# Optimization experiments

Hardware: AMD Instinct MI355X
Metric: run time of the kernel (lower is better)

Reference implementation:

```python
import jax, jax.numpy as jnp
import numpy as np

N_NODES = 50000
N_EDGES = 800000
F_IN = 128
HID = 128
F_ADD = 32
N_GRAPHS = 128


def setup_inputs() -> dict:
    key = jax.random.key(0)
    ks = jax.random.split(key, 12)
    x = jax.random.normal(ks[0], (N_NODES, F_IN), dtype=jnp.float32)
    edge_index = jax.random.randint(ks[1], (2, N_EDGES), 0, N_NODES, dtype=jnp.int64)
    batch = jnp.sort(jax.random.randint(ks[2], (N_NODES,), 0, N_GRAPHS, dtype=jnp.int64))
    additional_features = jax.random.normal(ks[3], (N_GRAPHS, F_ADD), dtype=jnp.float32)
    def glorot(k, shape):
        fan_in, fan_out = shape[0], shape[1]
        lim = jnp.sqrt(6.0 / (fan_in + fan_out)).astype(jnp.float32)
        return jax.random.uniform(k, shape, jnp.float32, -lim, lim)
    W1 = glorot(ks[4], (F_IN, HID)); b1 = jnp.zeros((HID,), jnp.float32)
    W2 = glorot(ks[5], (HID, HID)); b2 = jnp.zeros((HID,), jnp.float32)
    fc1_w = glorot(ks[6], (HID + F_ADD, HID)); fc1_b = jnp.zeros((HID,), jnp.float32)
    fc2_w = glorot(ks[7], (HID, 2)); fc2_b = jnp.zeros((2,), jnp.float32)
    return {"x": x, "edge_index": edge_index, "batch": batch,
            "additional_features": additional_features,
            "W1": W1, "b1": b1, "W2": W2, "b2": b2,
            "fc1_w": fc1_w, "fc1_b": fc1_b, "fc2_w": fc2_w, "fc2_b": fc2_b}


def _gcn_conv(h, src, dst, norm, W, b):
    # h: [N, d_in]; symmetric-normalized scatter-add aggregation (PyG GCNConv)
    h = h @ W                                   # [N, d_out]
    msg = h[src] * norm[:, None]                # gather + scale: [E+N, d_out]
    return jax.ops.segment_sum(msg, dst, num_segments=N_NODES) + b


def reference(x, edge_index, batch, additional_features,
              W1, b1, W2, b2, fc1_w, fc1_b, fc2_w, fc2_b):
    loops = jnp.arange(N_NODES, dtype=edge_index.dtype)
    src = jnp.concatenate([edge_index[0], loops])   # A + I
    dst = jnp.concatenate([edge_index[1], loops])
    deg = jax.ops.segment_sum(jnp.ones_like(src, dtype=x.dtype), dst,
                              num_segments=N_NODES)
    dinv = jnp.where(deg > 0, jax.lax.rsqrt(jnp.maximum(deg, 1.0)), 0.0)
    norm = dinv[src] * dinv[dst]

    h = jax.nn.relu(_gcn_conv(x, src, dst, norm, W1, b1))
    h = jax.nn.relu(_gcn_conv(h, src, dst, norm, W2, b2))
    # dropout is identity in eval mode

    sums = jax.ops.segment_sum(h, batch, num_segments=N_GRAPHS)    # [G, HID]
    counts = jax.ops.segment_sum(jnp.ones((N_NODES,), h.dtype), batch,
                                 num_segments=N_GRAPHS)
    pooled = sums / jnp.maximum(counts, 1.0)[:, None]              # global_mean_pool

    z = jnp.concatenate([pooled, additional_features], axis=1)     # [G, HID+F_ADD]
    z = jax.nn.relu(z @ fc1_w + fc1_b)
    return z @ fc2_w + fc2_b                                       # [G, 2]
```

## Files before the change

kernel.cpp:

```cpp
#include <hip/hip_runtime.h>

#define NN 50000
#define NE 800000
#define FD 128
#define FDH 64
#define FA 32
#define NG 128
#define EETOT (NE + NN)
#define NBLK ((NN + 255) / 256)
#define NPXCD 6250
#define ECHK 2048
#define NCHK ((NE + ECHK - 1) / ECHK)
#define FPB 52
#define FILLB (8 * FPB)
#define GEMMB ((NN + 63) / 64)

typedef __attribute__((ext_vector_type(8))) short short8;
typedef __attribute__((ext_vector_type(4))) float f32x4;

__device__ __forceinline__ float bfbits(unsigned short u) {
    return __uint_as_float(((unsigned int)u) << 16);
}
__device__ __forceinline__ float bflo(unsigned int p) { return __uint_as_float(p << 16); }
__device__ __forceinline__ float bfhi(unsigned int p) { return __uint_as_float(p & 0xffff0000u); }
__device__ __forceinline__ unsigned short f2bf(float f) {
    unsigned int u = __float_as_uint(f);
    unsigned int r = u + 0x7FFFu + ((u >> 16) & 1u);
    return (unsigned short)(r >> 16);
}
__device__ __forceinline__ unsigned int packbf(float a, float b) {
    return (unsigned int)f2bf(a) | ((unsigned int)f2bf(b) << 16);
}

__device__ __forceinline__ int wave_probe_bf16(const unsigned int* t, int nwords) {
    int lane = threadIdx.x & 63;
    unsigned int wv = (lane < nwords) ? t[lane] : 0u;
    int nzp = (wv != 0u) ? 1 : 0;
    unsigned int e = (wv >> 7) & 0xFFu;
    int hitp = (nzp && e >= 100u && e <= 140u) ? 1 : 0;
    int nz = __popcll(__ballot(nzp));
    int hits = __popcll(__ballot(hitp));
    return (nz < 8) ? 1 : (hits * 4 >= nz * 3);
}
__device__ __forceinline__ int wave_probe_is64(const int* ei) {
    int lane = threadIdx.x & 63;
    int v = (lane < 32) ? ei[2 * lane + 1] : 0;
    return (__ballot(v != 0) == 0ull) ? 1 : 0;
}

__global__ __launch_bounds__(128) void mark_kernel(float* out, float v) {
    out[threadIdx.x] = v;
}

__global__ __launch_bounds__(256) void prep(
        const void* addf, const void* w1, const void* b1, const void* w2,
        const void* b2, const void* fc1w, const void* fc1b, const void* fc2w,
        const void* fc2b, unsigned int* W1t, unsigned int* W2t,
        float* addff, float* b1f, float* b2f, float* fc1wf, float* fc1bf,
        float* fc2wf, float* fc2bf, int* degi, int* tsum) {
    int b = blockIdx.x;
    if (b < 64) {
        int rel = b * 256 + threadIdx.x;
        const void* src = (rel < 8192) ? w1 : w2;
        unsigned int* dst = (rel < 8192) ? W1t : W2t;
        int flag = wave_probe_bf16((const unsigned int*)src, 64);
        int rr = rel & 8191;
        int n = rr >> 6, kk = rr & 63;
        float lo, hi;
        if (flag) {
            const unsigned short* s = (const unsigned short*)src;
            lo = bfbits(s[(2 * kk) * FD + n]);
            hi = bfbits(s[(2 * kk + 1) * FD + n]);
        } else {
            const float* s = (const float*)src;
            lo = s[(2 * kk) * FD + n];
            hi = s[(2 * kk + 1) * FD + n];
        }
        dst[rr] = packbf(lo, hi);
    } else if (b < 163) {
        int i = (b - 64) * 256 + threadIdx.x;
        int wb = (b - 64) * 256 + (threadIdx.x & ~63);
        const void* src; float* dst; int base; int prnw; int lim;
        if      (wb < 4096)  { src = addf; dst = addff; base = 0;     prnw = 64; lim = 4096;  }
        else if (wb < 4224)  { src = b1;   dst = b1f;   base = 4096;  prnw = 64; lim = 128;   }
        else if (wb < 4352)  { src = b2;   dst = b2f;   base = 4224;  prnw = 64; lim = 128;   }
        else if (wb < 24832) { src = fc1w; dst = fc1wf; base = 4352;  prnw = 64; lim = 20480; }
        else if (wb < 24960) { src = fc1b; dst = fc1bf; base = 24832; prnw = 64; lim = 128;   }
        else if (wb < 25216) { src = fc2w; dst = fc2wf; base = 24960; prnw = 64; lim = 256;   }
        else if (wb < 25280) { src = fc2b; dst = fc2bf; base = 25216; prnw = 1;  lim = 2;     }
        else return;
        int flag = wave_probe_bf16((const unsigned int*)src, prnw);
        int rel = i - base;
        if (rel < lim) {
            if (flag) dst[rel] = bfbits(((const unsigned short*)src)[rel]);
            else      dst[rel] = ((const float*)src)[rel];
        }
    } else {
        int i = (b - 163) * 256 + threadIdx.x;
        if      (i < NN)       degi[i] = 0;
        else if (i < NN + 256) tsum[i - NN] = 0;
    }
}

__global__ __launch_bounds__(256) void bin_gemm1(const int* ei, int* deg,
        int2* ebsd, int* bofs,
        const void* __restrict__ Av, const unsigned int* __restrict__ Wt,
        unsigned short* __restrict__ C) {
    __shared__ unsigned int hA[64][68];
    if ((int)blockIdx.x < NCHK) {
        __shared__ int cnt[8];
        __shared__ int sbase[8];
        int is64 = wave_probe_is64(ei);
        int chunk = blockIdx.x;
        int e0 = chunk * ECHK;
        int nedge = NE - e0; if (nedge > ECHK) nedge = ECHK;
        if (threadIdx.x < 8) cnt[threadIdx.x] = 0;
        __syncthreads();
        int sA[8], dA[8], rk[8], pr[8];
        #pragma unroll
        for (int k = 0; k < 8; ++k) {
            int j = k * 256 + threadIdx.x;
            pr[k] = -1;
            if (j < nedge) {
                int e = e0 + j;
                int s = is64 ? ei[2 * e] : ei[e];
                int d = is64 ? ei[2 * (NE + e)] : ei[NE + e];
                atomicAdd(&deg[d], 1);
                int p = d / NPXCD;
                sA[k] = s; dA[k] = d; pr[k] = p;
                rk[k] = atomicAdd(&cnt[p], 1);
            }
        }
        __syncthreads();
        if (threadIdx.x == 0) {
            int acc = 0;
            #pragma unroll
            for (int p = 0; p < 8; ++p) {
                sbase[p] = acc;
                bofs[chunk * 8 + p] = acc;
                acc += cnt[p];
            }
        }
        __syncthreads();
        #pragma unroll
        for (int k = 0; k < 8; ++k) {
            if (pr[k] >= 0) {
                int idx = chunk * ECHK + sbase[pr[k]] + rk[k];
                ebsd[idx] = make_int2(sA[k], dA[k]);
            }
        }
        return;
    }
    int bid = blockIdx.x - NCHK;
    int mbase = bid * 64;
    bool f32in = !wave_probe_bf16((const unsigned int*)Av, 64);
    if (!f32in) {
        const unsigned int* xb = (const unsigned int*)Av;
        for (int i = threadIdx.x; i < 64 * 64; i += 256) {
            int row = i >> 6, w = i & 63;
            int gr = mbase + row; if (gr >= NN) gr = NN - 1;
            hA[row][w] = xb[(size_t)gr * 64 + w];
        }
    } else {
        const float2* xf2 = (const float2*)Av;
        for (int i = threadIdx.x; i < 64 * 64; i += 256) {
            int row = i >> 6, w = i & 63;
            int gr = mbase + row; if (gr >= NN) gr = NN - 1;
            float2 f = xf2[(size_t)gr * 64 + w];
            hA[row][w] = packbf(f.x, f.y);
        }
    }
    __syncthreads();
    int wave = threadIdx.x >> 6;
    int lane = threadIdx.x & 63;
    int quad = lane >> 4;
    int l16  = lane & 15;
    int lrow = wave * 16 + l16;
    short8 af[4];
    #pragma unroll
    for (int kk = 0; kk < 4; ++kk) {
        uint4 v = *(const uint4*)&hA[lrow][(kk * 4 + quad) * 4];
        af[kk] = *(short8*)&v;
    }
    __syncthreads();
    f32x4 accs[8];
    #pragma unroll
    for (int nt = 0; nt < 8; ++nt) {
        int n = nt * 16 + l16;
        const uint4* Wrow = (const uint4*)(Wt + (size_t)n * FDH);
        f32x4 acc = {0.f, 0.f, 0.f, 0.f};
        #pragma unroll
        for (int kk = 0; kk < 4; ++kk) {
            uint4 wv = Wrow[kk * 4 + quad];
            short8 bf = *(short8*)&wv;
            acc = __builtin_amdgcn_mfma_f32_16x16x32_bf16(af[kk], bf, acc, 0, 0, 0);
        }
        accs[nt] = acc;
    }
    unsigned short* hs = (unsigned short*)hA;
    #pragma unroll
    for (int nt = 0; nt < 8; ++nt) {
        #pragma unroll
        for (int reg = 0; reg < 4; ++reg) {
            int row = wave * 16 + quad * 4 + reg;
            hs[row * 136 + nt * 16 + l16] = f2bf(accs[nt][reg]);
        }
    }
    __syncthreads();
    for (int i = threadIdx.x; i < 64 * 32; i += 256) {
        int row = i >> 5, q = i & 31;
        int gr = mbase + row;
        if (gr < NN)
            ((uint2*)C)[(size_t)gr * 32 + q] = ((const uint2*)&hs[row * 136])[q];
    }
}

__global__ __launch_bounds__(256) void scan_fused(const int* degi, const int* batch,
        int* tsum, float* dinv, int* rowstart, int* cursor, int* gstart) {
    __shared__ int sh[256];
    int b = blockIdx.x, t = threadIdx.x;
    int i = b * 256 + t;
    int d = (i < NN) ? degi[i] : 0;
    if (i < NN) dinv[i] = rsqrtf((float)(d + 1));
    int v = (i < NN) ? d + 1 : 0;
    sh[t] = v;
    __syncthreads();
    for (int off = 1; off < 256; off <<= 1) {
        int a = (t >= off) ? sh[t - off] : 0;
        __syncthreads();
        sh[t] += a;
        __syncthreads();
    }
    int incl = sh[t];
    int total = sh[255];
    if (t == 0) atomicExch(&tsum[b], total);
    int pt = 0;
    for (int j = t; j < b; j += 256) {
        int s;
        do { s = atomicAdd(&tsum[j], 0); } while (s == 0);
        pt += s;
    }
    __syncthreads();
    sh[t] = pt;
    __syncthreads();
    for (int off = 128; off >= 1; off >>= 1) {
        if (t < off) sh[t] += sh[t + off];
        __syncthreads();
    }
    int boff = sh[0];
    if (i < NN) {
        int r = boff + incl - v;
        rowstart[i] = r;
        cursor[i]   = r;
    }
    if (i == 0) rowstart[NN] = EETOT;
    if (i < NN) {
        int is64 = (batch[NN - 1] == 0) ? 1 : 0;
        int bc = is64 ? batch[2 * i] : batch[i];
        if (i == 0) {
            for (int g = 0; g <= bc; ++g) gstart[g] = 0;
        } else {
            int bp = is64 ? batch[2 * (i - 1)] : batch[i - 1];
            for (int g = bp + 1; g <= bc; ++g) gstart[g] = i;
        }
        if (i == NN - 1) {
            for (int g = bc + 1; g <= NG; ++g) gstart[g] = NN;
        }
    }
}

__global__ __launch_bounds__(256) void fill_kernel(const int2* ebsd, const int* bofs,
        const float* dinv, int* cursor, unsigned int* cv) {
    int par = blockIdx.x & 7;
    int g   = blockIdx.x >> 3;
    for (int chunk = g; chunk < NCHK; chunk += FPB) {
        int b0 = bofs[chunk * 8 + par];
        int nedge = NE - chunk * ECHK; if (nedge > ECHK) nedge = ECHK;
        int b1 = (par < 7) ? bofs[chunk * 8 + par + 1] : nedge;
        for (int j = b0 + (int)threadIdx.x; j < b1; j += 256) {
            int2 sd = ebsd[chunk * ECHK + j];
            int pos = atomicAdd(&cursor[sd.y], 1);
            cv[pos] = (unsigned int)sd.x
                    | ((unsigned int)f2bf(dinv[sd.x] * dinv[sd.y]) << 16);
        }
    }
    for (int n = par * NPXCD + g * 256 + threadIdx.x; n < (par + 1) * NPXCD;
         n += FPB * 256) {
        int pos = atomicAdd(&cursor[n], 1);
        float di = dinv[n];
        cv[pos] = (unsigned int)n | ((unsigned int)f2bf(di * di) << 16);
    }
}

__global__ __launch_bounds__(256) void agg_gemm2(const unsigned int* Hb,
        const unsigned int* cv, const int* rowstart, const float* bias,
        const unsigned int* __restrict__ Wt, unsigned short* __restrict__ C) {
    __shared__ unsigned int hA[16][68];
    int lane = threadIdx.x & 63;
    int r4   = lane >> 4;
    int c4   = lane & 15;
    int wv   = threadIdx.x >> 6;
    int nb = blockIdx.x * 16;
    int n = nb + wv * 4 + r4;
    const uint4* H4 = (const uint4*)Hb;
    int jb = rowstart[n], je = rowstart[n + 1];
    float a0 = 0.f, a1 = 0.f, a2 = 0.f, a3 = 0.f;
    float a4 = 0.f, a5 = 0.f, a6 = 0.f, a7 = 0.f;
    int j = jb;
    for (; j + 7 < je; j += 8) {
        unsigned int rr[8]; uint4 hh[8];
        #pragma unroll
        for (int k = 0; k < 8; ++k) rr[k] = cv[j + k];
        #pragma unroll
        for (int k = 0; k < 8; ++k) hh[k] = H4[(size_t)(rr[k] & 0xFFFFu) * 16 + c4];
        #pragma unroll
        for (int k = 0; k < 8; ++k) {
            float v = bfbits((unsigned short)(rr[k] >> 16));
            a0 += v * bflo(hh[k].x); a1 += v * bfhi(hh[k].x);
            a2 += v * bflo(hh[k].y); a3 += v * bfhi(hh[k].y);
            a4 += v * bflo(hh[k].z); a5 += v * bfhi(hh[k].z);
            a6 += v * bflo(hh[k].w); a7 += v * bfhi(hh[k].w);
        }
    }
    for (; j + 3 < je; j += 4) {
        unsigned int rr[4]; uint4 hh[4];
        #pragma unroll
        for (int k = 0; k < 4; ++k) rr[k] = cv[j + k];
        #pragma unroll
        for (int k = 0; k < 4; ++k) hh[k] = H4[(size_t)(rr[k] & 0xFFFFu) * 16 + c4];
        #pragma unroll
        for (int k = 0; k < 4; ++k) {
            float v = bfbits((unsigned short)(rr[k] >> 16));
            a0 += v * bflo(hh[k].x); a1 += v * bfhi(hh[k].x);
            a2 += v * bflo(hh[k].y); a3 += v * bfhi(hh[k].y);
            a4 += v * bflo(hh[k].z); a5 += v * bfhi(hh[k].z);
            a6 += v * bflo(hh[k].w); a7 += v * bfhi(hh[k].w);
        }
    }
    for (; j < je; ++j) {
        unsigned int r = cv[j];
        uint4 h = H4[(size_t)(r & 0xFFFFu) * 16 + c4];
        float v = bfbits((unsigned short)(r >> 16));
        a0 += v * bflo(h.x); a1 += v * bfhi(h.x);
        a2 += v * bflo(h.y); a3 += v * bfhi(h.y);
        a4 += v * bflo(h.z); a5 += v * bfhi(h.z);
        a6 += v * bflo(h.w); a7 += v * bfhi(h.w);
    }
    a0 = fmaxf(a0 + bias[8 * c4 + 0], 0.f);
    a1 = fmaxf(a1 + bias[8 * c4 + 1], 0.f);
    a2 = fmaxf(a2 + bias[8 * c4 + 2], 0.f);
    a3 = fmaxf(a3 + bias[8 * c4 + 3], 0.f);
    a4 = fmaxf(a4 + bias[8 * c4 + 4], 0.f);
    a5 = fmaxf(a5 + bias[8 * c4 + 5], 0.f);
    a6 = fmaxf(a6 + bias[8 * c4 + 6], 0.f);
    a7 = fmaxf(a7 + bias[8 * c4 + 7], 0.f);
    int lrow = wv * 4 + r4;
    hA[lrow][c4 * 4 + 0] = packbf(a0, a1);
    hA[lrow][c4 * 4 + 1] = packbf(a2, a3);
    hA[lrow][c4 * 4 + 2] = packbf(a4, a5);
    hA[lrow][c4 * 4 + 3] = packbf(a6, a7);
    __syncthreads();
    int quad = lane >> 4;
    int l16  = lane & 15;
    short8 af[4];
    #pragma unroll
    for (int kk = 0; kk < 4; ++kk) {
        const uint4* p = (const uint4*)&hA[l16][(kk * 4 + quad) * 4];
        uint4 v = *p;
        af[kk] = *(short8*)&v;
    }
    #pragma unroll
    for (int t = 0; t < 2; ++t) {
        int nt = wv * 2 + t;
        int nn2 = nt * 16 + l16;
        const uint4* Wrow = (const uint4*)(Wt + (size_t)nn2 * FDH);
        f32x4 acc = {0.f, 0.f, 0.f, 0.f};
        #pragma unroll
        for (int kk = 0; kk < 4; ++kk) {
            uint4 wvv = Wrow[kk * 4 + quad];
            short8 bf = *(short8*)&wvv;
            acc = __builtin_amdgcn_mfma_f32_16x16x32_bf16(af[kk], bf, acc, 0, 0, 0);
        }
        int row0 = nb + quad * 4;
        #pragma unroll
        for (int reg = 0; reg < 4; ++reg) {
            int r = row0 + reg;
            C[(size_t)r * FD + nt * 16 + l16] = f2bf(acc[reg]);
        }
    }
}

__global__ __launch_bounds__(256) void aggregate_kernel(const unsigned int* Hb,
        const unsigned int* cv, const int* rowstart, const float* bias,
        unsigned int* outb) {
    int lane = threadIdx.x & 63;
    int r4   = lane >> 4;
    int c4   = lane & 15;
    int wv   = threadIdx.x >> 6;
    int n = blockIdx.x * 16 + wv * 4 + r4;
    const uint4* H4 = (const uint4*)Hb;
    int jb = rowstart[n], je = rowstart[n + 1];
    float a0 = 0.f, a1 = 0.f, a2 = 0.f, a3 = 0.f;
    float a4 = 0.f, a5 = 0.f, a6 = 0.f, a7 = 0.f;
    int j = jb;
    for (; j + 7 < je; j += 8) {
        unsigned int rr[8]; uint4 hh[8];
        #pragma unroll
        for (int k = 0; k < 8; ++k) rr[k] = cv[j + k];
        #pragma unroll
        for (int k = 0; k < 8; ++k) hh[k] = H4[(size_t)(rr[k] & 0xFFFFu) * 16 + c4];
        #pragma unroll
        for (int k = 0; k < 8; ++k) {
            float v = bfbits((unsigned short)(rr[k] >> 16));
            a0 += v * bflo(hh[k].x); a1 += v * bfhi(hh[k].x);
            a2 += v * bflo(hh[k].y); a3 += v * bfhi(hh[k].y);
            a4 += v * bflo(hh[k].z); a5 += v * bfhi(hh[k].z);
            a6 += v * bflo(hh[k].w); a7 += v * bfhi(hh[k].w);
        }
    }
    for (; j + 3 < je; j += 4) {
        unsigned int rr[4]; uint4 hh[4];
        #pragma unroll
        for (int k = 0; k < 4; ++k) rr[k] = cv[j + k];
        #pragma unroll
        for (int k = 0; k < 4; ++k) hh[k] = H4[(size_t)(rr[k] & 0xFFFFu) * 16 + c4];
        #pragma unroll
        for (int k = 0; k < 4; ++k) {
            float v = bfbits((unsigned short)(rr[k] >> 16));
            a0 += v * bflo(hh[k].x); a1 += v * bfhi(hh[k].x);
            a2 += v * bflo(hh[k].y); a3 += v * bfhi(hh[k].y);
            a4 += v * bflo(hh[k].z); a5 += v * bfhi(hh[k].z);
            a6 += v * bflo(hh[k].w); a7 += v * bfhi(hh[k].w);
        }
    }
    for (; j < je; ++j) {
        unsigned int r = cv[j];
        uint4 h = H4[(size_t)(r & 0xFFFFu) * 16 + c4];
        float v = bfbits((unsigned short)(r >> 16));
        a0 += v * bflo(h.x); a1 += v * bfhi(h.x);
        a2 += v * bflo(h.y); a3 += v * bfhi(h.y);
        a4 += v * bflo(h.z); a5 += v * bfhi(h.z);
        a6 += v * bflo(h.w); a7 += v * bfhi(h.w);
    }
    a0 = fmaxf(a0 + bias[8 * c4 + 0], 0.f);
    a1 = fmaxf(a1 + bias[8 * c4 + 1], 0.f);
    a2 = fmaxf(a2 + bias[8 * c4 + 2], 0.f);
    a3 = fmaxf(a3 + bias[8 * c4 + 3], 0.f);
    a4 = fmaxf(a4 + bias[8 * c4 + 4], 0.f);
    a5 = fmaxf(a5 + bias[8 * c4 + 5], 0.f);
    a6 = fmaxf(a6 + bias[8 * c4 + 6], 0.f);
    a7 = fmaxf(a7 + bias[8 * c4 + 7], 0.f);
    uint4 out;
    out.x = packbf(a0, a1);
    out.y = packbf(a2, a3);
    out.z = packbf(a4, a5);
    out.w = packbf(a6, a7);
    ((uint4*)outb)[(size_t)n * 16 + c4] = out;
}

__global__ __launch_bounds__(256) void poolhead(const unsigned int* Hb,
        const int* gstart, const float* addf, const float* fc1w, const float* fc1b,
        const float* fc2w, const float* fc2b, const unsigned int* x, void* outp) {
    int g = blockIdx.x;
    int t = threadIdx.x;
    int q = t >> 6, w = t & 63;
    int obf = wave_probe_bf16(x, 64);
    int s = gstart[g], e = gstart[g + 1];
    float a0 = 0.f, a1 = 0.f;
    #pragma unroll 4
    for (int n = s + q; n < e; n += 4) {
        unsigned int h = Hb[(size_t)n * FDH + w];
        a0 += bflo(h);
        a1 += bfhi(h);
    }
    __shared__ float pp[4][FD];
    __shared__ float z[FD + FA];
    __shared__ float h[FD];
    pp[q][2 * w]     = a0;
    pp[q][2 * w + 1] = a1;
    __syncthreads();
    if (t < FD) {
        float cnt = (float)(e - s);
        if (cnt < 1.0f) cnt = 1.0f;
        z[t] = (pp[0][t] + pp[1][t] + pp[2][t] + pp[3][t]) / cnt;
    }
    if (t >= FD && t < FD + FA) z[t] = addf[g * FA + (t - FD)];
    __syncthreads();
    if (t < FD) {
        float acc = fc1b[t];
        #pragma unroll 4
        for (int k = 0; k < FD + FA; ++k)
            acc += z[k] * fc1w[k * FD + t];
        h[t] = fmaxf(acc, 0.f);
    }
    __syncthreads();
    if (t < 2) {
        float o = fc2b[t];
        for (int j = 0; j < FD; ++j) o += h[j] * fc2w[j * 2 + t];
        if (obf) ((unsigned short*)outp)[g * 2 + t] = f2bf(o);
        else     ((float*)outp)[g * 2 + t] = o;
    }
}

extern "C" void kernel_launch(void* const* d_in, const int* in_sizes, int n_in,
                              void* d_out, int out_size, void* d_ws, size_t ws_size,
                              hipStream_t stream) {
    (void)out_size;

    if (n_in != 12) {
        hipLaunchKernelGGL(mark_kernel, dim3(1), dim3(128), 0, stream,
                           (float*)d_out, 2000.0f);
        return;
    }
    const int exp_sizes[12] = {6400000, 1600000, 50000, 4096, 16384, 128,
                               16384, 128, 20480, 128, 256, 2};
    for (int i = 0; i < 12; ++i) {
        if (in_sizes[i] != exp_sizes[i]) {
            hipLaunchKernelGGL(mark_kernel, dim3(1), dim3(128), 0, stream,
                               (float*)d_out, 3000.0f + 100.0f * i);
            return;
        }
    }

    size_t off = 0;
    char* base = (char*)d_ws;
#define WSALLOC(ptr, type, nbytes) \
    type* ptr = (type*)(base + off); off += (((size_t)(nbytes)) + 255) & ~(size_t)255;
    WSALLOC(bufA,  unsigned int, (size_t)NN * FDH * 4)
    WSALLOC(bufB,  unsigned int, (size_t)NN * FDH * 4)
    WSALLOC(dinv,  float, (size_t)NN * 4)
    WSALLOC(degi,  int,   (size_t)NN * 4)
    WSALLOC(tsum,  int,   256 * 4)
    WSALLOC(rowst, int,   (size_t)(NN + 1) * 4)
    WSALLOC(cursor,int,   (size_t)NN * 4)
    WSALLOC(cv,    unsigned int, (size_t)EETOT * 4)
    WSALLOC(gstart,int,   (size_t)(NG + 1) * 4)
    WSALLOC(ebsd,  int2,  (size_t)NCHK * ECHK * 8)
    WSALLOC(bofs,  int,   (size_t)NCHK * 8 * 4)
    WSALLOC(W1t,   unsigned int, (size_t)FD * FDH * 4)
    WSALLOC(W2t,   unsigned int, (size_t)FD * FDH * 4)
    WSALLOC(b1f,   float, FD * 4)
    WSALLOC(b2f,   float, FD * 4)
    WSALLOC(addff, float, (size_t)NG * FA * 4)
    WSALLOC(fc1wf, float, (size_t)(FD + FA) * FD * 4)
    WSALLOC(fc1bf, float, FD * 4)
    WSALLOC(fc2wf, float, FD * 2 * 4)
    WSALLOC(fc2bf, float, 2 * 4)
#undef WSALLOC
    if (ws_size < off) {
        hipLaunchKernelGGL(mark_kernel, dim3(1), dim3(128), 0, stream,
                           (float*)d_out, 1000.0f);
        return;
    }

    const int* ei    = (const int*)d_in[1];
    const int* batch = (const int*)d_in[2];

    hipLaunchKernelGGL(prep, dim3(360), dim3(256), 0, stream,
                       d_in[3], d_in[4], d_in[5], d_in[6], d_in[7],
                       d_in[8], d_in[9], d_in[10], d_in[11],
                       W1t, W2t, addff, b1f, b2f, fc1wf, fc1bf,
                       fc2wf, fc2bf, degi, tsum);

    hipLaunchKernelGGL(bin_gemm1, dim3(NCHK + GEMMB), dim3(256), 0, stream,
                       ei, degi, ebsd, bofs,
                       d_in[0], W1t, (unsigned short*)bufA);

    hipLaunchKernelGGL(scan_fused, dim3(NBLK), dim3(256), 0, stream,
                       degi, batch, tsum, dinv, rowst, cursor, gstart);

    hipLaunchKernelGGL(fill_kernel, dim3(FILLB), dim3(256), 0, stream,
                       ebsd, bofs, dinv, cursor, cv);

    hipLaunchKernelGGL(agg_gemm2, dim3(NN / 16), dim3(256), 0, stream,
                       bufA, cv, rowst, b1f, W2t, (unsigned short*)bufB);

    hipLaunchKernelGGL(aggregate_kernel, dim3(NN / 16), dim3(256), 0, stream,
                       bufB, cv, rowst, b2f, bufA);

    hipLaunchKernelGGL(poolhead, dim3(NG), dim3(256), 0, stream,
                       bufA, gstart, addff, fc1wf, fc1bf, fc2wf, fc2bf,
                       (const unsigned int*)d_in[0], d_out);
}
```

Before: 278.8 us.

## Move edge binning into prep kernel and count degrees from binned edges

Edge binning by destination partition now runs inside the prep kernel, and the degree histogram moves into the GEMM1 kernel. There, blocks walk the binned edge list one destination partition at a time, so each block's degree atomics land in a narrow, likely cache-local range instead of random addresses across all nodes. The cost is an extra read of the binned edge array in the second kernel. The prep launch also grows by the binning blocks, and the degree counters are zeroed in the same launch before the second kernel reads them.

```diff
diff --git a/kernel.cpp b/kernel.cpp
--- a/kernel.cpp
+++ b/kernel.cpp
@@ -14,6 +14,7 @@
 #define FPB 52
 #define FILLB (8 * FPB)
 #define GEMMB ((NN + 63) / 64)
+#define PREPB 360
 
 typedef __attribute__((ext_vector_type(8))) short short8;
 typedef __attribute__((ext_vector_type(4))) float f32x4;
@@ -52,12 +53,13 @@
     out[threadIdx.x] = v;
 }
 
-__global__ __launch_bounds__(256) void prep(
+__global__ __launch_bounds__(256) void prep_bin(
         const void* addf, const void* w1, const void* b1, const void* w2,
         const void* b2, const void* fc1w, const void* fc1b, const void* fc2w,
         const void* fc2b, unsigned int* W1t, unsigned int* W2t,
         float* addff, float* b1f, float* b2f, float* fc1wf, float* fc1bf,
-        float* fc2wf, float* fc2bf, int* degi, int* tsum) {
+        float* fc2wf, float* fc2bf, int* degi, int* tsum,
+        const int* ei, int2* ebsd, int* bofs) {
     int b = blockIdx.x;
     if (b < 64) {
         int rel = b * 256 + threadIdx.x;
@@ -77,6 +79,7 @@
             hi = s[(2 * kk + 1) * FD + n];
         }
         dst[rr] = packbf(lo, hi);
+        return;
     } else if (b < 163) {
         int i = (b - 64) * 256 + threadIdx.x;
         int wb = (b - 64) * 256 + (threadIdx.x & ~63);
@@ -95,63 +98,75 @@
             if (flag) dst[rel] = bfbits(((const unsigned short*)src)[rel]);
             else      dst[rel] = ((const float*)src)[rel];
         }
-    } else {
+        return;
+    } else if (b < PREPB) {
         int i = (b - 163) * 256 + threadIdx.x;
         if      (i < NN)       degi[i] = 0;
         else if (i < NN + 256) tsum[i - NN] = 0;
-    }
-}
-
-__global__ __launch_bounds__(256) void bin_gemm1(const int* ei, int* deg,
-        int2* ebsd, int* bofs,
+        return;
+    }
+    __shared__ int cnt[8];
+    __shared__ int sbase[8];
+    int is64 = wave_probe_is64(ei);
+    int chunk = b - PREPB;
+    int e0 = chunk * ECHK;
+    int nedge = NE - e0; if (nedge > ECHK) nedge = ECHK;
+    if (threadIdx.x < 8) cnt[threadIdx.x] = 0;
+    __syncthreads();
+    int sA[8], dA[8], rk[8], pr[8];
+    #pragma unroll
+    for (int k = 0; k < 8; ++k) {
+        int j = k * 256 + threadIdx.x;
+        pr[k] = -1;
+        if (j < nedge) {
+            int e = e0 + j;
+            int s = is64 ? ei[2 * e] : ei[e];
+            int d = is64 ? ei[2 * (NE + e)] : ei[NE + e];
+            int p = d / NPXCD;
+            sA[k] = s; dA[k] = d; pr[k] = p;
+            rk[k] = atomicAdd(&cnt[p], 1);
+        }
+    }
+    __syncthreads();
+    if (threadIdx.x == 0) {
+        int acc = 0;
+        #pragma unroll
+        for (int p = 0; p < 8; ++p) {
+            sbase[p] = acc;
+            bofs[chunk * 8 + p] = acc;
+            acc += cnt[p];
+        }
+    }
+    __syncthreads();
+    #pragma unroll
+    for (int k = 0; k < 8; ++k) {
+        if (pr[k] >= 0) {
+            int idx = chunk * ECHK + sbase[pr[k]] + rk[k];
+            ebsd[idx] = make_int2(sA[k], dA[k]);
+        }
+    }
+}
+
+__global__ __launch_bounds__(256) void deg_gemm1(const int2* ebsd, const int* bofs,
+        int* degi,
         const void* __restrict__ Av, const unsigned int* __restrict__ Wt,
         unsigned short* __restrict__ C) {
     __shared__ unsigned int hA[64][68];
-    if ((int)blockIdx.x < NCHK) {
-        __shared__ int cnt[8];
-        __shared__ int sbase[8];
-        int is64 = wave_probe_is64(ei);
-        int chunk = blockIdx.x;
-        int e0 = chunk * ECHK;
-        int nedge = NE - e0; if (nedge > ECHK) nedge = ECHK;
-        if (threadIdx.x < 8) cnt[threadIdx.x] = 0;
-        __syncthreads();
-        int sA[8], dA[8], rk[8], pr[8];
-        #pragma unroll
-        for (int k = 0; k < 8; ++k) {
-            int j = k * 256 + threadIdx.x;
-            pr[k] = -1;
-            if (j < nedge) {
-                int e = e0 + j;
-                int s = is64 ? ei[2 * e] : ei[e];
-                int d = is64 ? ei[2 * (NE + e)] : ei[NE + e];
-                atomicAdd(&deg[d], 1);
-                int p = d / NPXCD;
-                sA[k] = s; dA[k] = d; pr[k] = p;
-                rk[k] = atomicAdd(&cnt[p], 1);
+    if ((int)blockIdx.x < FILLB) {
+        int par = blockIdx.x & 7;
+        int g   = blockIdx.x >> 3;
+        for (int chunk = g; chunk < NCHK; chunk += FPB) {
+            int b0 = bofs[chunk * 8 + par];
+            int nedge = NE - chunk * ECHK; if (nedge > ECHK) nedge = ECHK;
+            int b1 = (par < 7) ? bofs[chunk * 8 + par + 1] : nedge;
+            for (int j = b0 + (int)threadIdx.x; j < b1; j += 256) {
+                int2 sd = ebsd[chunk * ECHK + j];
+                atomicAdd(&degi[sd.y], 1);
             }
         }
-        __syncthreads();
-        if (threadIdx.x == 0) {
-            int acc = 0;
-            #pragma unroll
-            for (int p = 0; p < 8; ++p) {
-                sbase[p] = acc;
-                bofs[chunk * 8 + p] = acc;
-                acc += cnt[p];
-            }
-        }
-        __syncthreads();
-        #pragma unroll
-        for (int k = 0; k < 8; ++k) {
-            if (pr[k] >= 0) {
-                int idx = chunk * ECHK + sbase[pr[k]] + rk[k];
-                ebsd[idx] = make_int2(sA[k], dA[k]);
-            }
-        }
         return;
     }
-    int bid = blockIdx.x - NCHK;
+    int bid = blockIdx.x - FILLB;
     int mbase = bid * 64;
     bool f32in = !wave_probe_bf16((const unsigned int*)Av, 64);
     if (!f32in) {
@@ -556,14 +571,14 @@
     const int* ei    = (const int*)d_in[1];
     const int* batch = (const int*)d_in[2];
 
-    hipLaunchKernelGGL(prep, dim3(360), dim3(256), 0, stream,
+    hipLaunchKernelGGL(prep_bin, dim3(PREPB + NCHK), dim3(256), 0, stream,
                        d_in[3], d_in[4], d_in[5], d_in[6], d_in[7],
                        d_in[8], d_in[9], d_in[10], d_in[11],
                        W1t, W2t, addff, b1f, b2f, fc1wf, fc1bf,
-                       fc2wf, fc2bf, degi, tsum);
-
-    hipLaunchKernelGGL(bin_gemm1, dim3(NCHK + GEMMB), dim3(256), 0, stream,
-                       ei, degi, ebsd, bofs,
+                       fc2wf, fc2bf, degi, tsum, ei, ebsd, bofs);
+
+    hipLaunchKernelGGL(deg_gemm1, dim3(FILLB + GEMMB), dim3(256), 0, stream,
+                       ebsd, bofs, degi,
                        d_in[0], W1t, (unsigned short*)bufA);
 
     hipLaunchKernelGGL(scan_fused, dim3(NBLK), dim3(256), 0, stream,
```

Result: no change. 275.1 us (-1.3%).
